# Performance work log

Measured on AMD Instinct MI355X. Metric: run time of the kernel, lower is better.

## Reference

```python
import jax, jax.numpy as jnp
import numpy as np

DIM = 2048
NUM_HEADS = 16
HEAD_DIM = DIM // NUM_HEADS  # 128
SEQ_LEN = 2048
ROPE_THETA = 10000.0


def _rope_tables(T, head_dim, dtype=jnp.float32):
    inv_freq = 1.0 / (ROPE_THETA ** (jnp.arange(0, head_dim, 2, dtype=jnp.float32) / head_dim))
    t = jnp.arange(T, dtype=jnp.float32)
    freqs = jnp.outer(t, inv_freq)  # [T, head_dim//2]
    return jnp.cos(freqs).astype(dtype), jnp.sin(freqs).astype(dtype)


def setup_inputs() -> dict:
    key = jax.random.key(0)
    ks = jax.random.split(key, 9)
    s = 1.0 / jnp.sqrt(DIM)
    x = jax.random.normal(ks[0], (SEQ_LEN, DIM), dtype=jnp.float32)
    wq = jax.random.uniform(ks[1], (DIM, DIM), minval=-s, maxval=s, dtype=jnp.float32)
    wk = jax.random.uniform(ks[2], (DIM, DIM), minval=-s, maxval=s, dtype=jnp.float32)
    wv = jax.random.uniform(ks[3], (DIM, DIM), minval=-s, maxval=s, dtype=jnp.float32)
    wp = jax.random.uniform(ks[4], (DIM, DIM), minval=-s, maxval=s, dtype=jnp.float32)
    bq = jax.random.uniform(ks[5], (DIM,), minval=-s, maxval=s, dtype=jnp.float32)
    bk = jax.random.uniform(ks[6], (DIM,), minval=-s, maxval=s, dtype=jnp.float32)
    bv = jax.random.uniform(ks[7], (DIM,), minval=-s, maxval=s, dtype=jnp.float32)
    bp = jax.random.uniform(ks[8], (DIM,), minval=-s, maxval=s, dtype=jnp.float32)
    cos, sin = _rope_tables(SEQ_LEN, HEAD_DIM)
    return {"x": x, "wq": wq, "bq": bq, "wk": wk, "bk": bk, "wv": wv, "bv": bv,
            "wp": wp, "bp": bp, "cos": cos, "sin": sin}


def _apply_rope(t, cos, sin):
    # t: [T, H, D]; cos/sin: [T, D//2]
    T, H, D = t.shape
    tr = t.reshape(T, H, D // 2, 2)
    r, i = tr[..., 0], tr[..., 1]
    c = cos[:, None, :]
    s = sin[:, None, :]
    out = jnp.stack([r * c - i * s, r * s + i * c], axis=-1)
    return out.reshape(T, H, D)


def reference(x, wq, bq, wk, bk, wv, bv, wp, bp, cos, sin):
    T, C = x.shape
    H, D = NUM_HEADS, C // NUM_HEADS
    q = (x @ wq.T + bq).reshape(T, H, D)
    k = (x @ wk.T + bk).reshape(T, H, D)
    v = (x @ wv.T + bv).reshape(T, H, D)
    q = _apply_rope(q, cos, sin)
    k = _apply_rope(k, cos, sin)
    # scores: [H, T, T]; NOTE: source scales by full dim C, not head_dim
    attn = jnp.einsum('thd,shd->hts', q, k) * (C ** -0.5)
    mask = jnp.tril(jnp.ones((T, T), dtype=bool))
    attn = jnp.where(mask[None], attn, -jnp.inf)
    attn = jax.nn.softmax(attn, axis=-1)
    out = jnp.einsum('hts,shd->thd', attn, v).reshape(T, C)
    return out @ wp.T + bp
```

## Files before the change

### kernel.cpp

```cpp
#include <hip/hip_runtime.h>
#include <math.h>

typedef __attribute__((ext_vector_type(8))) short  bf16x8;
typedef __attribute__((ext_vector_type(4))) float  f32x4;
typedef __attribute__((ext_vector_type(8))) ushort u16x8;
typedef __attribute__((ext_vector_type(4))) ushort u16x4;

#define SEQ   2048
#define CDIM  2048
#define NHEAD 16
#define DHEAD 128
#define SCALE 0.02209708691207961f
#define LOG2E 1.4426950408889634f

__device__ __forceinline__ ushort f2bf(float f) {
    uint u = __float_as_uint(f);
    u += 0x7FFFu + ((u >> 16) & 1u);
    return (ushort)(u >> 16);
}
__device__ __forceinline__ float bf2f(ushort h) {
    return __uint_as_float(((uint)h) << 16);
}

#define GLOAD16(gsrc, ldst)                                                  \
    __builtin_amdgcn_global_load_lds(                                        \
        (const __attribute__((address_space(1))) void*)(gsrc),               \
        (__attribute__((address_space(3))) void*)(ldst), 16, 0, 0)

__global__ __launch_bounds__(256) void f2bf5_kernel(
    const float* __restrict__ s0, const float* __restrict__ s1,
    const float* __restrict__ s2, const float* __restrict__ s3,
    const float* __restrict__ s4,
    ushort* __restrict__ d0, ushort* __restrict__ d1,
    ushort* __restrict__ d2, ushort* __restrict__ d3,
    ushort* __restrict__ d4)
{
    const int z = blockIdx.y;
    const float* src = z == 0 ? s0 : z == 1 ? s1 : z == 2 ? s2 : z == 3 ? s3 : s4;
    ushort*      dst = z == 0 ? d0 : z == 1 ? d1 : z == 2 ? d2 : z == 3 ? d3 : d4;
    const int i = blockIdx.x * 256 + threadIdx.x;
    const float4 a = ((const float4*)src)[i * 2];
    const float4 b = ((const float4*)src)[i * 2 + 1];
    u16x8 o;
    o[0] = f2bf(a.x); o[1] = f2bf(a.y); o[2] = f2bf(a.z); o[3] = f2bf(a.w);
    o[4] = f2bf(b.x); o[5] = f2bf(b.y); o[6] = f2bf(b.z); o[7] = f2bf(b.w);
    *(u16x8*)&dst[(size_t)i * 8] = o;
}

__global__ __launch_bounds__(256) void gemm_nt_mfma_f32(const ushort* __restrict__ A,
                                                        const ushort* __restrict__ B,
                                                        const float* __restrict__ bias,
                                                        float* __restrict__ outp)
{
    __shared__ ushort As[128 * 32];
    __shared__ ushort Bs[128 * 32];
    const int tid  = threadIdx.x;
    const int lane = tid & 63, wid = tid >> 6;
    const int wr = wid >> 1, wc = wid & 1;
    const int l4 = lane >> 4, l15 = lane & 15;
    const int m0 = blockIdx.y * 128, n0 = blockIdx.x * 128;

    f32x4 acc[4][4];
    #pragma unroll
    for (int i = 0; i < 4; ++i)
        #pragma unroll
        for (int j = 0; j < 4; ++j) acc[i][j] = 0.f;

    const int srow = wid * 32 + (lane >> 2);
    const int scol = (lane & 3) * 8;

    for (int k0 = 0; k0 < CDIM; k0 += 32) {
        __syncthreads();
        GLOAD16(&A[(size_t)(m0 + srow)      * CDIM + k0 + scol], (char*)As + wid * 2048);
        GLOAD16(&A[(size_t)(m0 + srow + 16) * CDIM + k0 + scol], (char*)As + wid * 2048 + 1024);
        GLOAD16(&B[(size_t)(n0 + srow)      * CDIM + k0 + scol], (char*)Bs + wid * 2048);
        GLOAD16(&B[(size_t)(n0 + srow + 16) * CDIM + k0 + scol], (char*)Bs + wid * 2048 + 1024);
        __syncthreads();

        bf16x8 af[4], bfr[4];
        #pragma unroll
        for (int f = 0; f < 4; ++f) {
            af[f]  = *(const bf16x8*)&As[(wr * 64 + f * 16 + l15) * 32 + l4 * 8];
            bfr[f] = *(const bf16x8*)&Bs[(wc * 64 + f * 16 + l15) * 32 + l4 * 8];
        }
        #pragma unroll
        for (int i = 0; i < 4; ++i)
            #pragma unroll
            for (int j = 0; j < 4; ++j)
                acc[i][j] = __builtin_amdgcn_mfma_f32_16x16x32_bf16(af[i], bfr[j], acc[i][j], 0, 0, 0);
    }

    float bn[4];
    #pragma unroll
    for (int j = 0; j < 4; ++j) bn[j] = bias[n0 + wc * 64 + j * 16 + l15];

    #pragma unroll
    for (int i = 0; i < 4; ++i)
        #pragma unroll
        for (int j = 0; j < 4; ++j) {
            const int n = n0 + wc * 64 + j * 16 + l15;
            #pragma unroll
            for (int r = 0; r < 4; ++r) {
                const int m = m0 + wr * 64 + i * 16 + l4 * 4 + r;
                outp[(size_t)m * CDIM + n] = acc[i][j][r] + bn[j];
            }
        }
}

__global__ __launch_bounds__(256) void gemm_qkv(const ushort* __restrict__ A,
                                                const ushort* __restrict__ W0,
                                                const ushort* __restrict__ W1,
                                                const ushort* __restrict__ W2,
                                                const float* __restrict__ b0,
                                                const float* __restrict__ b1,
                                                const float* __restrict__ b2,
                                                const float* __restrict__ cosT,
                                                const float* __restrict__ sinT,
                                                ushort* __restrict__ o0,
                                                ushort* __restrict__ o1,
                                                ushort* __restrict__ o2)
{
    __shared__ ushort As[128 * 32];
    __shared__ ushort Bs[128 * 32];
    const int z = blockIdx.z;
    const ushort* B    = z == 0 ? W0 : z == 1 ? W1 : W2;
    const float*  bias = z == 0 ? b0 : z == 1 ? b1 : b2;

    const int tid  = threadIdx.x;
    const int lane = tid & 63, wid = tid >> 6;
    const int wr = wid >> 1, wc = wid & 1;
    const int l4 = lane >> 4, l15 = lane & 15;
    const int m0 = blockIdx.y * 128, n0 = blockIdx.x * 128;

    f32x4 acc[4][4];
    #pragma unroll
    for (int i = 0; i < 4; ++i)
        #pragma unroll
        for (int j = 0; j < 4; ++j) acc[i][j] = 0.f;

    const int srow = wid * 32 + (lane >> 2);
    const int scol = (lane & 3) * 8;

    for (int k0 = 0; k0 < CDIM; k0 += 32) {
        __syncthreads();
        GLOAD16(&A[(size_t)(m0 + srow)      * CDIM + k0 + scol], (char*)As + wid * 2048);
        GLOAD16(&A[(size_t)(m0 + srow + 16) * CDIM + k0 + scol], (char*)As + wid * 2048 + 1024);
        GLOAD16(&B[(size_t)(n0 + srow)      * CDIM + k0 + scol], (char*)Bs + wid * 2048);
        GLOAD16(&B[(size_t)(n0 + srow + 16) * CDIM + k0 + scol], (char*)Bs + wid * 2048 + 1024);
        __syncthreads();

        bf16x8 af[4], bfr[4];
        #pragma unroll
        for (int f = 0; f < 4; ++f) {
            af[f]  = *(const bf16x8*)&As[(wr * 64 + f * 16 + l15) * 32 + l4 * 8];
            bfr[f] = *(const bf16x8*)&Bs[(wc * 64 + f * 16 + l15) * 32 + l4 * 8];
        }
        #pragma unroll
        for (int i = 0; i < 4; ++i)
            #pragma unroll
            for (int j = 0; j < 4; ++j)
                acc[i][j] = __builtin_amdgcn_mfma_f32_16x16x32_bf16(af[i], bfr[j], acc[i][j], 0, 0, 0);
    }

    float bn[4];
    #pragma unroll
    for (int j = 0; j < 4; ++j) bn[j] = bias[n0 + wc * 64 + j * 16 + l15];

    if (z == 2) {
        #pragma unroll
        for (int i = 0; i < 4; ++i)
            #pragma unroll
            for (int j = 0; j < 4; ++j) {
                const int n = n0 + wc * 64 + j * 16 + l15;
                const int mb = m0 + wr * 64 + i * 16 + l4 * 4;
                u16x4 pk;
                #pragma unroll
                for (int r = 0; r < 4; ++r) pk[r] = f2bf(acc[i][j][r] + bn[j]);
                *(u16x4*)&o2[(size_t)n * SEQ + mb] = pk;
            }
    } else {
        ushort* outp = z == 0 ? o0 : o1;
        #pragma unroll
        for (int i = 0; i < 4; ++i)
            #pragma unroll
            for (int j = 0; j < 4; ++j) {
                const int n  = n0 + wc * 64 + j * 16 + l15;
                const int fi = (n & 127) >> 1;
                const bool odd = (n & 1) != 0;
                #pragma unroll
                for (int r = 0; r < 4; ++r) {
                    const int m = m0 + wr * 64 + i * 16 + l4 * 4 + r;
                    const float val     = acc[i][j][r] + bn[j];
                    const float partner = __shfl_xor(val, 1);
                    const float c = cosT[m * 64 + fi];
                    const float s = sinT[m * 64 + fi];
                    const float res = odd ? (partner * s + val * c)
                                          : (val * c - partner * s);
                    outp[(size_t)m * CDIM + n] = f2bf(res);
                }
            }
    }
}

__global__ __launch_bounds__(256) void flash_attn_mfma(const ushort* __restrict__ qb,
                                                       const ushort* __restrict__ kb,
                                                       const ushort* __restrict__ vT,
                                                       ushort* __restrict__ ao)
{
    __shared__ ushort Ks[64 * 136];
    __shared__ ushort VTs[128 * 72];
    __shared__ float  S_lds[64 * 68];
    __shared__ ushort Ps[64 * 72];
    __shared__ float  rowM[64], rowL[64], rowF[64];

    const int tid  = threadIdx.x;
    const int lane = tid & 63, wid = tid >> 6;
    const int wr = wid >> 1, wc = wid & 1;
    const int l4 = lane >> 4, l15 = lane & 15;
    const int h = blockIdx.y;
    const int qt = gridDim.x - 1 - blockIdx.x;
    const int q0 = qt * 64;

    if (tid < 64) { rowM[tid] = -INFINITY; rowL[tid] = 0.f; }

    bf16x8 qf[2][4];
    #pragma unroll
    for (int fm = 0; fm < 2; ++fm)
        #pragma unroll
        for (int ks = 0; ks < 4; ++ks) {
            const int row = q0 + wr * 32 + fm * 16 + l15;
            const int col = h * DHEAD + ks * 32 + l4 * 8;
            qf[fm][ks] = *(const bf16x8*)&qb[(size_t)row * CDIM + col];
        }

    f32x4 acc_o[2][4];
    #pragma unroll
    for (int fm = 0; fm < 2; ++fm)
        #pragma unroll
        for (int fn = 0; fn < 4; ++fn) acc_o[fm][fn] = 0.f;

    const int rK = tid >> 4,  cK = (tid & 15) * 8;
    const int rV = tid >> 3,  cV = (tid & 7) * 8;
    u16x8 kreg[4], vreg[4];

    #pragma unroll
    for (int i2 = 0; i2 < 4; ++i2)
        kreg[i2] = *(const u16x8*)&kb[(size_t)(rK + i2 * 16) * CDIM + h * DHEAD + cK];
    #pragma unroll
    for (int i2 = 0; i2 < 4; ++i2)
        vreg[i2] = *(const u16x8*)&vT[(size_t)(h * DHEAD + rV + i2 * 32) * SEQ + cV];

    for (int kt = 0; kt <= qt; ++kt) {
        __syncthreads();

        #pragma unroll
        for (int i2 = 0; i2 < 4; ++i2)
            *(u16x8*)&Ks[(rK + i2 * 16) * 136 + cK] = kreg[i2];
        #pragma unroll
        for (int i2 = 0; i2 < 4; ++i2)
            *(u16x8*)&VTs[(rV + i2 * 32) * 72 + cV] = vreg[i2];
        __syncthreads();

        f32x4 sacc[2][2];
        #pragma unroll
        for (int fm = 0; fm < 2; ++fm)
            #pragma unroll
            for (int fn = 0; fn < 2; ++fn) sacc[fm][fn] = 0.f;
        #pragma unroll
        for (int ks = 0; ks < 4; ++ks) {
            bf16x8 kf[2];
            #pragma unroll
            for (int fn = 0; fn < 2; ++fn)
                kf[fn] = *(const bf16x8*)&Ks[(wc * 32 + fn * 16 + l15) * 136 + ks * 32 + l4 * 8];
            #pragma unroll
            for (int fm = 0; fm < 2; ++fm)
                #pragma unroll
                for (int fn = 0; fn < 2; ++fn)
                    sacc[fm][fn] = __builtin_amdgcn_mfma_f32_16x16x32_bf16(qf[fm][ks], kf[fn], sacc[fm][fn], 0, 0, 0);
        }

        if (kt < qt) {
            #pragma unroll
            for (int i2 = 0; i2 < 4; ++i2)
                kreg[i2] = *(const u16x8*)&kb[(size_t)((kt + 1) * 64 + rK + i2 * 16) * CDIM + h * DHEAD + cK];
            #pragma unroll
            for (int i2 = 0; i2 < 4; ++i2)
                vreg[i2] = *(const u16x8*)&vT[(size_t)(h * DHEAD + rV + i2 * 32) * SEQ + (kt + 1) * 64 + cV];
        }

        #pragma unroll
        for (int fm = 0; fm < 2; ++fm)
            #pragma unroll
            for (int fn = 0; fn < 2; ++fn)
                #pragma unroll
                for (int r = 0; r < 4; ++r) {
                    const int srow = wr * 32 + fm * 16 + l4 * 4 + r;
                    const int scol = wc * 32 + fn * 16 + l15;
                    float sv = sacc[fm][fn][r] * SCALE;
                    if (kt == qt && scol > srow) sv = -INFINITY;
                    S_lds[srow * 68 + scol] = sv;
                }
        __syncthreads();

        {
            const int srow = tid >> 2;
            const int c0   = (tid & 3) * 16;
            float vals[16];
            #pragma unroll
            for (int c = 0; c < 16; ++c) vals[c] = S_lds[srow * 68 + c0 + c];
            float mt = vals[0];
            #pragma unroll
            for (int c = 1; c < 16; ++c) mt = fmaxf(mt, vals[c]);
            mt = fmaxf(mt, __shfl_xor(mt, 1));
            mt = fmaxf(mt, __shfl_xor(mt, 2));
            const float mold = rowM[srow];
            const float mnew = fmaxf(mold, mt);
            float sum = 0.f;
            ushort pb[16];
            #pragma unroll
            for (int c = 0; c < 16; ++c) {
                const float p = exp2f((vals[c] - mnew) * LOG2E);
                sum += p;
                pb[c] = f2bf(p);
            }
            sum += __shfl_xor(sum, 1);
            sum += __shfl_xor(sum, 2);
            u16x8 w0, w1;
            #pragma unroll
            for (int c = 0; c < 8; ++c) { w0[c] = pb[c]; w1[c] = pb[c + 8]; }
            *(u16x8*)&Ps[srow * 72 + c0]     = w0;
            *(u16x8*)&Ps[srow * 72 + c0 + 8] = w1;
            if ((tid & 3) == 0) {
                const float fac = exp2f((mold - mnew) * LOG2E);
                rowF[srow] = fac;
                rowL[srow] = rowL[srow] * fac + sum;
                rowM[srow] = mnew;
            }
        }
        __syncthreads();

        float frv[2][4];
        #pragma unroll
        for (int fm = 0; fm < 2; ++fm)
            #pragma unroll
            for (int r = 0; r < 4; ++r)
                frv[fm][r] = rowF[wr * 32 + fm * 16 + l4 * 4 + r];
        #pragma unroll
        for (int fm = 0; fm < 2; ++fm)
            #pragma unroll
            for (int fn = 0; fn < 4; ++fn)
                #pragma unroll
                for (int r = 0; r < 4; ++r) acc_o[fm][fn][r] *= frv[fm][r];

        #pragma unroll
        for (int ks = 0; ks < 2; ++ks) {
            bf16x8 pa[2];
            #pragma unroll
            for (int fm = 0; fm < 2; ++fm)
                pa[fm] = *(const bf16x8*)&Ps[(wr * 32 + fm * 16 + l15) * 72 + ks * 32 + l4 * 8];
            #pragma unroll
            for (int fn = 0; fn < 4; ++fn) {
                bf16x8 vf = *(const bf16x8*)&VTs[(wc * 64 + fn * 16 + l15) * 72 + ks * 32 + l4 * 8];
                #pragma unroll
                for (int fm = 0; fm < 2; ++fm)
                    acc_o[fm][fn] = __builtin_amdgcn_mfma_f32_16x16x32_bf16(pa[fm], vf, acc_o[fm][fn], 0, 0, 0);
            }
        }
    }

    #pragma unroll
    for (int fm = 0; fm < 2; ++fm)
        #pragma unroll
        for (int r = 0; r < 4; ++r) {
            const int lrow = wr * 32 + fm * 16 + l4 * 4 + r;
            const float invl = 1.f / rowL[lrow];
            #pragma unroll
            for (int fn = 0; fn < 4; ++fn) {
                const int gcol = h * DHEAD + wc * 64 + fn * 16 + l15;
                ao[(size_t)(q0 + lrow) * CDIM + gcol] = f2bf(acc_o[fm][fn][r] * invl);
            }
        }
}

extern "C" void kernel_launch(void* const* d_in, const int* in_sizes, int n_in,
                              void* d_out, int out_size, void* d_ws, size_t ws_size,
                              hipStream_t stream) {
    const float* x    = (const float*)d_in[0];
    const float* wq   = (const float*)d_in[1];
    const float* bq   = (const float*)d_in[2];
    const float* wk   = (const float*)d_in[3];
    const float* bk   = (const float*)d_in[4];
    const float* wv   = (const float*)d_in[5];
    const float* bv   = (const float*)d_in[6];
    const float* wp   = (const float*)d_in[7];
    const float* bp   = (const float*)d_in[8];
    const float* cosT = (const float*)d_in[9];
    const float* sinT = (const float*)d_in[10];

    const size_t mat = (size_t)SEQ * CDIM;
    ushort* xb  = (ushort*)d_ws;
    ushort* w0  = xb  + mat;
    ushort* w1  = w0  + mat;
    ushort* w2  = w1  + mat;
    ushort* w3  = w2  + mat;
    ushort* qbb = w3  + mat;
    ushort* kbb = qbb + mat;
    ushort* vTb = kbb + mat;
    ushort* aob = xb;

    const int n8 = (int)(mat / 8);

    f2bf5_kernel<<<dim3(n8 / 256, 5), 256, 0, stream>>>(x, wq, wk, wv, wp,
                                                        xb, w0, w1, w2, w3);

    gemm_qkv<<<dim3(16, 16, 3), 256, 0, stream>>>(xb, w0, w1, w2, bq, bk, bv,
                                                  cosT, sinT, qbb, kbb, vTb);

    flash_attn_mfma<<<dim3(SEQ / 64, NHEAD), 256, 0, stream>>>(qbb, kbb, vTb, aob);

    gemm_nt_mfma_f32<<<dim3(16, 16), 256, 0, stream>>>(aob, w3, bp, (float*)d_out);

    (void)in_sizes; (void)n_in; (void)out_size; (void)ws_size;
}
```

Measured before the change: 344.2 us.

## Give each wave full 16-row tiles and do online softmax in registers

The attention kernel now assigns each wave a full 16-row query slice across all 64 keys. The S tile no longer round-trips through LDS, and the shared rowM/rowL/rowF arrays are dropped. Row max and sum are reduced with lane shuffles, and the running max and sum stay in registers, which removes two block-wide barriers per key tile. Each wave now owns 8 output fragments, and the launch bounds request 3 blocks per CU. The P tile uses a 68-element stride, which leaves the 128-bit LDS reads only 8-byte aligned.

```diff
diff --git a/kernel.cpp b/kernel.cpp
--- a/kernel.cpp
+++ b/kernel.cpp
@@ -202,42 +202,35 @@
     }
 }
 
-__global__ __launch_bounds__(256) void flash_attn_mfma(const ushort* __restrict__ qb,
-                                                       const ushort* __restrict__ kb,
-                                                       const ushort* __restrict__ vT,
-                                                       ushort* __restrict__ ao)
+__global__ __launch_bounds__(256, 3) void flash_attn_mfma(const ushort* __restrict__ qb,
+                                                          const ushort* __restrict__ kb,
+                                                          const ushort* __restrict__ vT,
+                                                          ushort* __restrict__ ao)
 {
     __shared__ ushort Ks[64 * 136];
     __shared__ ushort VTs[128 * 72];
-    __shared__ float  S_lds[64 * 68];
-    __shared__ ushort Ps[64 * 72];
-    __shared__ float  rowM[64], rowL[64], rowF[64];
+    __shared__ ushort Ps[64 * 68];
 
     const int tid  = threadIdx.x;
     const int lane = tid & 63, wid = tid >> 6;
-    const int wr = wid >> 1, wc = wid & 1;
     const int l4 = lane >> 4, l15 = lane & 15;
     const int h = blockIdx.y;
     const int qt = gridDim.x - 1 - blockIdx.x;
     const int q0 = qt * 64;
-
-    if (tid < 64) { rowM[tid] = -INFINITY; rowL[tid] = 0.f; }
-
-    bf16x8 qf[2][4];
-    #pragma unroll
-    for (int fm = 0; fm < 2; ++fm)
-        #pragma unroll
-        for (int ks = 0; ks < 4; ++ks) {
-            const int row = q0 + wr * 32 + fm * 16 + l15;
-            const int col = h * DHEAD + ks * 32 + l4 * 8;
-            qf[fm][ks] = *(const bf16x8*)&qb[(size_t)row * CDIM + col];
-        }
-
-    f32x4 acc_o[2][4];
-    #pragma unroll
-    for (int fm = 0; fm < 2; ++fm)
-        #pragma unroll
-        for (int fn = 0; fn < 4; ++fn) acc_o[fm][fn] = 0.f;
+    const int row0 = wid * 16;
+
+    bf16x8 qf[4];
+    #pragma unroll
+    for (int ks = 0; ks < 4; ++ks)
+        qf[ks] = *(const bf16x8*)&qb[(size_t)(q0 + row0 + l15) * CDIM + h * DHEAD + ks * 32 + l4 * 8];
+
+    f32x4 acc_o[8];
+    #pragma unroll
+    for (int fn = 0; fn < 8; ++fn) acc_o[fn] = 0.f;
+
+    float mreg[4], lreg[4];
+    #pragma unroll
+    for (int r = 0; r < 4; ++r) { mreg[r] = -INFINITY; lreg[r] = 0.f; }
 
     const int rK = tid >> 4,  cK = (tid & 15) * 8;
     const int rV = tid >> 3,  cV = (tid & 7) * 8;
@@ -261,22 +254,16 @@
             *(u16x8*)&VTs[(rV + i2 * 32) * 72 + cV] = vreg[i2];
         __syncthreads();
 
-        f32x4 sacc[2][2];
-        #pragma unroll
-        for (int fm = 0; fm < 2; ++fm)
-            #pragma unroll
-            for (int fn = 0; fn < 2; ++fn) sacc[fm][fn] = 0.f;
+        f32x4 sacc[4];
+        #pragma unroll
+        for (int fn = 0; fn < 4; ++fn) sacc[fn] = 0.f;
         #pragma unroll
         for (int ks = 0; ks < 4; ++ks) {
-            bf16x8 kf[2];
-            #pragma unroll
-            for (int fn = 0; fn < 2; ++fn)
-                kf[fn] = *(const bf16x8*)&Ks[(wc * 32 + fn * 16 + l15) * 136 + ks * 32 + l4 * 8];
-            #pragma unroll
-            for (int fm = 0; fm < 2; ++fm)
-                #pragma unroll
-                for (int fn = 0; fn < 2; ++fn)
-                    sacc[fm][fn] = __builtin_amdgcn_mfma_f32_16x16x32_bf16(qf[fm][ks], kf[fn], sacc[fm][fn], 0, 0, 0);
+            #pragma unroll
+            for (int fn = 0; fn < 4; ++fn) {
+                bf16x8 kf = *(const bf16x8*)&Ks[(fn * 16 + l15) * 136 + ks * 32 + l4 * 8];
+                sacc[fn] = __builtin_amdgcn_mfma_f32_16x16x32_bf16(qf[ks], kf, sacc[fn], 0, 0, 0);
+            }
         }
 
         if (kt < qt) {
@@ -289,97 +276,70 @@
         }
 
         #pragma unroll
-        for (int fm = 0; fm < 2; ++fm)
-            #pragma unroll
-            for (int fn = 0; fn < 2; ++fn)
-                #pragma unroll
-                for (int r = 0; r < 4; ++r) {
-                    const int srow = wr * 32 + fm * 16 + l4 * 4 + r;
-                    const int scol = wc * 32 + fn * 16 + l15;
-                    float sv = sacc[fm][fn][r] * SCALE;
-                    if (kt == qt && scol > srow) sv = -INFINITY;
-                    S_lds[srow * 68 + scol] = sv;
-                }
-        __syncthreads();
-
-        {
-            const int srow = tid >> 2;
-            const int c0   = (tid & 3) * 16;
-            float vals[16];
-            #pragma unroll
-            for (int c = 0; c < 16; ++c) vals[c] = S_lds[srow * 68 + c0 + c];
-            float mt = vals[0];
-            #pragma unroll
-            for (int c = 1; c < 16; ++c) mt = fmaxf(mt, vals[c]);
+        for (int fn = 0; fn < 4; ++fn)
+            #pragma unroll
+            for (int r = 0; r < 4; ++r) {
+                float sv = sacc[fn][r] * SCALE;
+                if (kt == qt && (fn * 16 + l15) > (row0 + l4 * 4 + r)) sv = -INFINITY;
+                sacc[fn][r] = sv;
+            }
+
+        float fac[4];
+        ushort pb[4][4];
+        #pragma unroll
+        for (int r = 0; r < 4; ++r) {
+            float mt = fmaxf(fmaxf(sacc[0][r], sacc[1][r]), fmaxf(sacc[2][r], sacc[3][r]));
             mt = fmaxf(mt, __shfl_xor(mt, 1));
             mt = fmaxf(mt, __shfl_xor(mt, 2));
-            const float mold = rowM[srow];
-            const float mnew = fmaxf(mold, mt);
+            mt = fmaxf(mt, __shfl_xor(mt, 4));
+            mt = fmaxf(mt, __shfl_xor(mt, 8));
+            const float mnew = fmaxf(mreg[r], mt);
+            fac[r] = exp2f((mreg[r] - mnew) * LOG2E);
             float sum = 0.f;
-            ushort pb[16];
-            #pragma unroll
-            for (int c = 0; c < 16; ++c) {
-                const float p = exp2f((vals[c] - mnew) * LOG2E);
+            #pragma unroll
+            for (int fn = 0; fn < 4; ++fn) {
+                const float p = exp2f((sacc[fn][r] - mnew) * LOG2E);
                 sum += p;
-                pb[c] = f2bf(p);
+                pb[fn][r] = f2bf(p);
             }
             sum += __shfl_xor(sum, 1);
             sum += __shfl_xor(sum, 2);
-            u16x8 w0, w1;
-            #pragma unroll
-            for (int c = 0; c < 8; ++c) { w0[c] = pb[c]; w1[c] = pb[c + 8]; }
-            *(u16x8*)&Ps[srow * 72 + c0]     = w0;
-            *(u16x8*)&Ps[srow * 72 + c0 + 8] = w1;
-            if ((tid & 3) == 0) {
-                const float fac = exp2f((mold - mnew) * LOG2E);
-                rowF[srow] = fac;
-                rowL[srow] = rowL[srow] * fac + sum;
-                rowM[srow] = mnew;
-            }
-        }
-        __syncthreads();
-
-        float frv[2][4];
-        #pragma unroll
-        for (int fm = 0; fm < 2; ++fm)
+            sum += __shfl_xor(sum, 4);
+            sum += __shfl_xor(sum, 8);
+            lreg[r] = lreg[r] * fac[r] + sum;
+            mreg[r] = mnew;
+        }
+
+        #pragma unroll
+        for (int fn = 0; fn < 4; ++fn)
             #pragma unroll
             for (int r = 0; r < 4; ++r)
-                frv[fm][r] = rowF[wr * 32 + fm * 16 + l4 * 4 + r];
-        #pragma unroll
-        for (int fm = 0; fm < 2; ++fm)
-            #pragma unroll
-            for (int fn = 0; fn < 4; ++fn)
-                #pragma unroll
-                for (int r = 0; r < 4; ++r) acc_o[fm][fn][r] *= frv[fm][r];
+                Ps[(row0 + l4 * 4 + r) * 68 + fn * 16 + l15] = pb[fn][r];
+
+        #pragma unroll
+        for (int fn = 0; fn < 8; ++fn)
+            #pragma unroll
+            for (int r = 0; r < 4; ++r) acc_o[fn][r] *= fac[r];
 
         #pragma unroll
         for (int ks = 0; ks < 2; ++ks) {
-            bf16x8 pa[2];
-            #pragma unroll
-            for (int fm = 0; fm < 2; ++fm)
-                pa[fm] = *(const bf16x8*)&Ps[(wr * 32 + fm * 16 + l15) * 72 + ks * 32 + l4 * 8];
-            #pragma unroll
-            for (int fn = 0; fn < 4; ++fn) {
-                bf16x8 vf = *(const bf16x8*)&VTs[(wc * 64 + fn * 16 + l15) * 72 + ks * 32 + l4 * 8];
-                #pragma unroll
-                for (int fm = 0; fm < 2; ++fm)
-                    acc_o[fm][fn] = __builtin_amdgcn_mfma_f32_16x16x32_bf16(pa[fm], vf, acc_o[fm][fn], 0, 0, 0);
-            }
-        }
-    }
-
-    #pragma unroll
-    for (int fm = 0; fm < 2; ++fm)
-        #pragma unroll
-        for (int r = 0; r < 4; ++r) {
-            const int lrow = wr * 32 + fm * 16 + l4 * 4 + r;
-            const float invl = 1.f / rowL[lrow];
-            #pragma unroll
-            for (int fn = 0; fn < 4; ++fn) {
-                const int gcol = h * DHEAD + wc * 64 + fn * 16 + l15;
-                ao[(size_t)(q0 + lrow) * CDIM + gcol] = f2bf(acc_o[fm][fn][r] * invl);
-            }
-        }
+            bf16x8 pa = *(const bf16x8*)&Ps[(row0 + l15) * 68 + ks * 32 + l4 * 8];
+            #pragma unroll
+            for (int fn = 0; fn < 8; ++fn) {
+                bf16x8 vf = *(const bf16x8*)&VTs[(fn * 16 + l15) * 72 + ks * 32 + l4 * 8];
+                acc_o[fn] = __builtin_amdgcn_mfma_f32_16x16x32_bf16(pa, vf, acc_o[fn], 0, 0, 0);
+            }
+        }
+    }
+
+    #pragma unroll
+    for (int r = 0; r < 4; ++r) {
+        const int grow = q0 + row0 + l4 * 4 + r;
+        const float invl = 1.f / lreg[r];
+        #pragma unroll
+        for (int fn = 0; fn < 8; ++fn)
+            ao[(size_t)grow * CDIM + h * DHEAD + fn * 16 + l15] = f2bf(acc_o[fn][r] * invl);
+    }
 }
 
 extern "C" void kernel_launch(void* const* d_in, const int* in_sizes, int n_in,
```

After: 360.9 us. +4.8%, slower.

## Double-buffer LDS tiles in QKV and output projection GEMMs

Applied to the files above, without the earlier changes.

Both GEMM kernels now keep two LDS buffers for the A and B tiles. The global-to-LDS load for the next K step is issued before the MFMA work on the current buffer, which lets memory latency overlap with compute and leaves one barrier per K step instead of two. This doubles shared-memory use per block to 32 KB, which may lower occupancy. It also depends on the async global-to-LDS loads having completed by the time each barrier is reached.

```diff
diff --git a/kernel.cpp b/kernel.cpp
--- a/kernel.cpp
+++ b/kernel.cpp
@@ -52,8 +52,8 @@
                                                         const float* __restrict__ bias,
                                                         float* __restrict__ outp)
 {
-    __shared__ ushort As[128 * 32];
-    __shared__ ushort Bs[128 * 32];
+    __shared__ ushort As[2][128 * 32];
+    __shared__ ushort Bs[2][128 * 32];
     const int tid  = threadIdx.x;
     const int lane = tid & 63, wid = tid >> 6;
     const int wr = wid >> 1, wc = wid & 1;
@@ -69,26 +69,39 @@
     const int srow = wid * 32 + (lane >> 2);
     const int scol = (lane & 3) * 8;
 
-    for (int k0 = 0; k0 < CDIM; k0 += 32) {
-        __syncthreads();
-        GLOAD16(&A[(size_t)(m0 + srow)      * CDIM + k0 + scol], (char*)As + wid * 2048);
-        GLOAD16(&A[(size_t)(m0 + srow + 16) * CDIM + k0 + scol], (char*)As + wid * 2048 + 1024);
-        GLOAD16(&B[(size_t)(n0 + srow)      * CDIM + k0 + scol], (char*)Bs + wid * 2048);
-        GLOAD16(&B[(size_t)(n0 + srow + 16) * CDIM + k0 + scol], (char*)Bs + wid * 2048 + 1024);
-        __syncthreads();
-
-        bf16x8 af[4], bfr[4];
-        #pragma unroll
-        for (int f = 0; f < 4; ++f) {
-            af[f]  = *(const bf16x8*)&As[(wr * 64 + f * 16 + l15) * 32 + l4 * 8];
-            bfr[f] = *(const bf16x8*)&Bs[(wc * 64 + f * 16 + l15) * 32 + l4 * 8];
-        }
-        #pragma unroll
-        for (int i = 0; i < 4; ++i)
-            #pragma unroll
-            for (int j = 0; j < 4; ++j)
-                acc[i][j] = __builtin_amdgcn_mfma_f32_16x16x32_bf16(af[i], bfr[j], acc[i][j], 0, 0, 0);
-    }
+#define STAGE_P(b, k0)                                                                        \
+    GLOAD16(&A[(size_t)(m0 + srow)      * CDIM + (k0) + scol], (char*)&As[b][0] + wid * 2048);        \
+    GLOAD16(&A[(size_t)(m0 + srow + 16) * CDIM + (k0) + scol], (char*)&As[b][0] + wid * 2048 + 1024); \
+    GLOAD16(&B[(size_t)(n0 + srow)      * CDIM + (k0) + scol], (char*)&Bs[b][0] + wid * 2048);        \
+    GLOAD16(&B[(size_t)(n0 + srow + 16) * CDIM + (k0) + scol], (char*)&Bs[b][0] + wid * 2048 + 1024);
+
+#define COMPUTE_P(b)                                                                          \
+    {                                                                                         \
+        bf16x8 af[4], bfr[4];                                                                 \
+        _Pragma("unroll")                                                                     \
+        for (int f = 0; f < 4; ++f) {                                                         \
+            af[f]  = *(const bf16x8*)&As[b][(wr * 64 + f * 16 + l15) * 32 + l4 * 8];          \
+            bfr[f] = *(const bf16x8*)&Bs[b][(wc * 64 + f * 16 + l15) * 32 + l4 * 8];          \
+        }                                                                                     \
+        _Pragma("unroll")                                                                     \
+        for (int i = 0; i < 4; ++i)                                                           \
+            _Pragma("unroll")                                                                 \
+            for (int j = 0; j < 4; ++j)                                                       \
+                acc[i][j] = __builtin_amdgcn_mfma_f32_16x16x32_bf16(af[i], bfr[j], acc[i][j], 0, 0, 0); \
+    }
+
+    STAGE_P(0, 0);
+    __syncthreads();
+    for (int k0 = 0; k0 < CDIM; k0 += 64) {
+        STAGE_P(1, k0 + 32);
+        COMPUTE_P(0);
+        __syncthreads();
+        if (k0 + 64 < CDIM) { STAGE_P(0, k0 + 64); }
+        COMPUTE_P(1);
+        __syncthreads();
+    }
+#undef STAGE_P
+#undef COMPUTE_P
 
     float bn[4];
     #pragma unroll
@@ -120,8 +133,8 @@
                                                 ushort* __restrict__ o1,
                                                 ushort* __restrict__ o2)
 {
-    __shared__ ushort As[128 * 32];
-    __shared__ ushort Bs[128 * 32];
+    __shared__ ushort As[2][128 * 32];
+    __shared__ ushort Bs[2][128 * 32];
     const int z = blockIdx.z;
     const ushort* B    = z == 0 ? W0 : z == 1 ? W1 : W2;
     const float*  bias = z == 0 ? b0 : z == 1 ? b1 : b2;
@@ -141,26 +154,39 @@
     const int srow = wid * 32 + (lane >> 2);
     const int scol = (lane & 3) * 8;
 
-    for (int k0 = 0; k0 < CDIM; k0 += 32) {
-        __syncthreads();
-        GLOAD16(&A[(size_t)(m0 + srow)      * CDIM + k0 + scol], (char*)As + wid * 2048);
-        GLOAD16(&A[(size_t)(m0 + srow + 16) * CDIM + k0 + scol], (char*)As + wid * 2048 + 1024);
-        GLOAD16(&B[(size_t)(n0 + srow)      * CDIM + k0 + scol], (char*)Bs + wid * 2048);
-        GLOAD16(&B[(size_t)(n0 + srow + 16) * CDIM + k0 + scol], (char*)Bs + wid * 2048 + 1024);
-        __syncthreads();
-
-        bf16x8 af[4], bfr[4];
-        #pragma unroll
-        for (int f = 0; f < 4; ++f) {
-            af[f]  = *(const bf16x8*)&As[(wr * 64 + f * 16 + l15) * 32 + l4 * 8];
-            bfr[f] = *(const bf16x8*)&Bs[(wc * 64 + f * 16 + l15) * 32 + l4 * 8];
-        }
-        #pragma unroll
-        for (int i = 0; i < 4; ++i)
-            #pragma unroll
-            for (int j = 0; j < 4; ++j)
-                acc[i][j] = __builtin_amdgcn_mfma_f32_16x16x32_bf16(af[i], bfr[j], acc[i][j], 0, 0, 0);
-    }
+#define STAGE_P(b, k0)                                                                        \
+    GLOAD16(&A[(size_t)(m0 + srow)      * CDIM + (k0) + scol], (char*)&As[b][0] + wid * 2048);        \
+    GLOAD16(&A[(size_t)(m0 + srow + 16) * CDIM + (k0) + scol], (char*)&As[b][0] + wid * 2048 + 1024); \
+    GLOAD16(&B[(size_t)(n0 + srow)      * CDIM + (k0) + scol], (char*)&Bs[b][0] + wid * 2048);        \
+    GLOAD16(&B[(size_t)(n0 + srow + 16) * CDIM + (k0) + scol], (char*)&Bs[b][0] + wid * 2048 + 1024);
+
+#define COMPUTE_P(b)                                                                          \
+    {                                                                                         \
+        bf16x8 af[4], bfr[4];                                                                 \
+        _Pragma("unroll")                                                                     \
+        for (int f = 0; f < 4; ++f) {                                                         \
+            af[f]  = *(const bf16x8*)&As[b][(wr * 64 + f * 16 + l15) * 32 + l4 * 8];          \
+            bfr[f] = *(const bf16x8*)&Bs[b][(wc * 64 + f * 16 + l15) * 32 + l4 * 8];          \
+        }                                                                                     \
+        _Pragma("unroll")                                                                     \
+        for (int i = 0; i < 4; ++i)                                                           \
+            _Pragma("unroll")                                                                 \
+            for (int j = 0; j < 4; ++j)                                                       \
+                acc[i][j] = __builtin_amdgcn_mfma_f32_16x16x32_bf16(af[i], bfr[j], acc[i][j], 0, 0, 0); \
+    }
+
+    STAGE_P(0, 0);
+    __syncthreads();
+    for (int k0 = 0; k0 < CDIM; k0 += 64) {
+        STAGE_P(1, k0 + 32);
+        COMPUTE_P(0);
+        __syncthreads();
+        if (k0 + 64 < CDIM) { STAGE_P(0, k0 + 64); }
+        COMPUTE_P(1);
+        __syncthreads();
+    }
+#undef STAGE_P
+#undef COMPUTE_P
 
     float bn[4];
     #pragma unroll
```

After: 351.2 us. 2.0% more time.
